# Kernel optimization log

Hardware: AMD Instinct MI355X
Metric: run time of the kernel (lower is better)

Reference implementation:

```python
import jax, jax.numpy as jnp
import numpy as np

B, N, H = 2048, 5, 5
IN, HID, OUT = 7, 2048, 512  # IN = 1 + c + c^2 with c = (H-1)//2 = 2


def setup_inputs() -> dict:
    key = jax.random.key(0)
    ks = jax.random.split(key, 7)
    k_in = 1.0 / np.sqrt(IN).astype(np.float32)
    k_h = 1.0 / np.sqrt(HID).astype(np.float32)
    return {
        "ins": jax.random.normal(ks[0], (B, N, H, H), jnp.float32),
        "w1": (jax.random.uniform(ks[1], (4, HID, IN), jnp.float32) - 0.5) * k_in,
        "b1": (jax.random.uniform(ks[2], (HID,), jnp.float32) - 0.5) * k_in,
        "w2": (jax.random.uniform(ks[3], (4, HID, HID), jnp.float32) - 0.5) * k_h,
        "b2": (jax.random.uniform(ks[4], (HID,), jnp.float32) - 0.5) * k_h,
        "w3": (jax.random.uniform(ks[5], (4, OUT, HID), jnp.float32) - 0.5) * k_h,
        "b3": (jax.random.uniform(ks[6], (OUT,), jnp.float32) - 0.5) * k_h,
        "ln_g": jnp.ones((HID,), jnp.float32),
        "ln_b": jnp.zeros((HID,), jnp.float32),
    }


def _rot90(x):
    # matches torch: x.flip(3).permute(0,1,3,2)
    return jnp.swapaxes(jnp.flip(x, axis=3), 2, 3)


def _orbit_stack(x):
    b, n = x.shape[0], x.shape[1]
    c = (x.shape[-1] - 1) // 2  # = 2 for H=5
    center = x[:, :, c, c]  # (B,N)
    parts = []
    xi = x
    for _ in range(4):  # fixed C4 group orbit, not a data loop
        parts.append(xi[:, :, :c, :c + 1].reshape(b, n, -1))  # (B,N,c+c^2)
        xi = _rot90(xi)
    orb = jnp.stack(parts, axis=-1)  # (B,N,c+c^2,4)
    cen = jnp.broadcast_to(center[..., None, None], (b, n, 1, 4))
    out = jnp.concatenate([cen, orb], axis=2)  # (B,N,n_orbits,4)
    return jnp.transpose(out, (0, 1, 3, 2))  # (B,N,4,n_orbits)


def _c4conv(w, bias, x):
    # block-circulant kernel: mat[g,h] = w[(h-g) % 4]
    mat = jnp.stack([jnp.roll(w, i, axis=0) for i in range(4)], axis=0)  # (4,4,out,in)
    return jnp.einsum('ghij,bnhj->bngi', mat, x) + bias


def _layernorm(x, g, b, eps=1e-5):
    m = jnp.mean(x, axis=-1, keepdims=True)
    v = jnp.mean(jnp.square(x - m), axis=-1, keepdims=True)
    return (x - m) / jnp.sqrt(v + eps) * g + b


def reference(ins, w1, b1, w2, b2, w3, b3, ln_g, ln_b):
    h = _orbit_stack(ins)                          # (B,N,4,7)
    h = jax.nn.relu(_c4conv(w1, b1, h))            # (B,N,4,HID)
    h = jax.nn.relu(_layernorm(_c4conv(w2, b2, h), ln_g, ln_b))
    return _c4conv(w3, b3, h)                      # (B,N,4,OUT)
```

## Files before the change

kernel.cpp:

```cpp
#include <hip/hip_runtime.h>
#include <stdint.h>


#define HID 2048
#define MROWS 10240

typedef float floatx4 __attribute__((ext_vector_type(4)));
typedef __bf16 bf16x8 __attribute__((ext_vector_type(8)));

__device__ __forceinline__ unsigned short f2bf(float f) {
  union { float f; unsigned int u; } v; v.f = f;
  unsigned int r = v.u + 0x7fffu + ((v.u >> 16) & 1u);
  return (unsigned short)(r >> 16);
}

template <int NO>
__global__ __launch_bounds__(256) void wtrans_kernel(const float* __restrict__ w,
                                                     unsigned short* __restrict__ W0s,
                                                     unsigned short* __restrict__ W2s,
                                                     unsigned short* __restrict__ Bc) {
  int idx = blockIdx.x * 256 + threadIdx.x;
  int i = idx >> 9, j4 = idx & 511;
  const float4* wp = (const float4*)w;
  float4 w0 = wp[0 * NO * 512 + i * 512 + j4];
  float4 w1 = wp[1 * NO * 512 + i * 512 + j4];
  float4 w2 = wp[2 * NO * 512 + i * 512 + j4];
  float4 w3 = wp[3 * NO * 512 + i * 512 + j4];
  ushort4 s0, s2, vr, vi, nvi;
#define DO(c)                                        \
  s0.c = f2bf(w0.c + w1.c + w2.c + w3.c);            \
  s2.c = f2bf(w0.c - w1.c + w2.c - w3.c);            \
  vr.c = f2bf(w0.c - w2.c);                          \
  vi.c = f2bf(w1.c - w3.c);                          \
  nvi.c = f2bf(-(w1.c - w3.c));
  DO(x) DO(y) DO(z) DO(w)
#undef DO
  ((ushort4*)W0s)[i * 512 + j4] = s0;
  ((ushort4*)W2s)[i * 512 + j4] = s2;
  ((ushort4*)Bc)[i * 1024 + j4] = vr;
  ((ushort4*)Bc)[i * 1024 + 512 + j4] = nvi;
  ((ushort4*)Bc)[(NO + i) * 1024 + j4] = vi;
  ((ushort4*)Bc)[(NO + i) * 1024 + 512 + j4] = vr;
}

__global__ __launch_bounds__(256) void layer1_kernel(const float* __restrict__ ins,
                                                     const float* __restrict__ w1,
                                                     const float* __restrict__ b1,
                                                     unsigned short* __restrict__ h1s,
                                                     int row0) {
  __shared__ float orbs[32][28];
  int t = threadIdx.x;
  int b0 = blockIdx.x * 32;
  int i = blockIdx.y * 256 + t;
  if (t < 32) {
    const float* x = ins + (size_t)(row0 + b0 + t) * 25;
    float v[25];
#pragma unroll
    for (int p = 0; p < 25; ++p) v[p] = x[p];
    float* o = orbs[t];
    o[0] = v[12]; o[7] = v[12]; o[14] = v[12]; o[21] = v[12];
#pragma unroll
    for (int r = 0; r < 2; ++r)
#pragma unroll
      for (int c = 0; c < 3; ++c) {
        int m = 1 + r * 3 + c;
        o[m]      = v[r * 5 + c];
        o[7 + m]  = v[c * 5 + (4 - r)];
        o[14 + m] = v[(4 - r) * 5 + (4 - c)];
        o[21 + m] = v[(4 - c) * 5 + r];
      }
  }
  __syncthreads();
  float w[4][7];
#pragma unroll
  for (int r = 0; r < 4; ++r)
#pragma unroll
    for (int j = 0; j < 7; ++j) w[r][j] = w1[(r * HID + i) * 7 + j];
  float bias = b1[i];
  for (int s = 0; s < 32; ++s) {
    float a[4] = {bias, bias, bias, bias};
#pragma unroll
    for (int hh = 0; hh < 4; ++hh)
#pragma unroll
      for (int j = 0; j < 7; ++j) {
        float ov = orbs[s][hh * 7 + j];
#pragma unroll
        for (int g = 0; g < 4; ++g) a[g] += w[(hh - g) & 3][j] * ov;
      }
    float h0 = fmaxf(a[0], 0.f), h1 = fmaxf(a[1], 0.f);
    float h2 = fmaxf(a[2], 0.f), h3 = fmaxf(a[3], 0.f);
    size_t base = (size_t)(b0 + s) * 8192 + i;
    h1s[base]        = f2bf(h0 + h1 + h2 + h3);
    h1s[base + 2048] = f2bf(h0 - h1 + h2 - h3);
    h1s[base + 4096] = f2bf(h0 - h2);
    h1s[base + 6144] = f2bf(h3 - h1);
  }
}

#define BM 128
#define BN 128
#define BK 64

__global__ __launch_bounds__(256) void gemm_spec(const unsigned short* __restrict__ A,
                                                 const unsigned short* __restrict__ B0,
                                                 const unsigned short* __restrict__ B1,
                                                 const unsigned short* __restrict__ B2,
                                                 float* __restrict__ C,
                                                 int s1, int s2, int N0, int ldc) {
  __shared__ __align__(16) unsigned short As[BM * BK];
  __shared__ __align__(16) unsigned short Bs[BN * BK];
  int tid = threadIdx.x;
  int wave = tid >> 6;
  int lane = tid & 63;
  int lane15 = lane & 15;
  int lane4 = lane >> 4;
  int m0 = blockIdx.y * BM;

  int bx = blockIdx.x;
  const unsigned short* Bp;
  int K, aoff, coff, nloc;
  if (bx < s1)      { Bp = B0; K = 2048; aoff = 0;    coff = 0;      nloc = bx * BN; }
  else if (bx < s2) { Bp = B1; K = 2048; aoff = 2048; coff = N0;     nloc = (bx - s1) * BN; }
  else              { Bp = B2; K = 4096; aoff = 4096; coff = 2 * N0; nloc = (bx - s2) * BN; }
  int ldb = K;

  int srow = wave * 8 + (lane >> 3);
  int scol = ((lane & 7) ^ (lane >> 3)) * 8;

  const unsigned short* Ag = A + (size_t)(m0 + srow) * 8192 + aoff + scol;
  const unsigned short* Bg = Bp + (size_t)(nloc + srow) * ldb + scol;

  int wm = (wave >> 1) * 64;
  int wn = (wave & 1) * 64;

  const floatx4 fz = {0.f, 0.f, 0.f, 0.f};
  floatx4 acc[4][4];
#pragma unroll
  for (int a = 0; a < 4; ++a)
#pragma unroll
    for (int b = 0; b < 4; ++b) acc[a][b] = fz;

  for (int k0 = 0; k0 < K; k0 += BK) {
#pragma unroll
    for (int q = 0; q < 4; ++q)
      __builtin_amdgcn_global_load_lds(
          (const __attribute__((address_space(1))) void*)(Ag + k0 + (size_t)q * 32 * 8192),
          (__attribute__((address_space(3))) void*)((char*)As + q * 4096 + wave * 1024),
          16, 0, 0);
#pragma unroll
    for (int q = 0; q < 4; ++q)
      __builtin_amdgcn_global_load_lds(
          (const __attribute__((address_space(1))) void*)(Bg + k0 + (size_t)q * 32 * ldb),
          (__attribute__((address_space(3))) void*)((char*)Bs + q * 4096 + wave * 1024),
          16, 0, 0);
    __syncthreads();
#pragma unroll
    for (int ks = 0; ks < 2; ++ks) {
      int chA = ((ks * 4 + lane4) ^ (lane15 & 7)) * 8;
      bf16x8 af[4], bfr[4];
#pragma unroll
      for (int mi = 0; mi < 4; ++mi)
        af[mi] = *(const bf16x8*)&As[(wm + mi * 16 + lane15) * BK + chA];
#pragma unroll
      for (int ni = 0; ni < 4; ++ni)
        bfr[ni] = *(const bf16x8*)&Bs[(wn + ni * 16 + lane15) * BK + chA];
#pragma unroll
      for (int mi = 0; mi < 4; ++mi)
#pragma unroll
        for (int ni = 0; ni < 4; ++ni)
          acc[mi][ni] = __builtin_amdgcn_mfma_f32_16x16x32_bf16(af[mi], bfr[ni], acc[mi][ni], 0, 0, 0);
    }
    __syncthreads();
  }

#pragma unroll
  for (int ni = 0; ni < 4; ++ni) {
    int col = coff + nloc + wn + ni * 16 + lane15;
#pragma unroll
    for (int mi = 0; mi < 4; ++mi) {
      int row = m0 + wm + mi * 16 + lane4 * 4;
#pragma unroll
      for (int r = 0; r < 4; ++r)
        C[(size_t)(row + r) * ldc + col] = acc[mi][ni][r];
    }
  }
}

__global__ __launch_bounds__(256) void ln_spec_kernel(const float* __restrict__ C2,
                                                      const float* __restrict__ b2,
                                                      const float* __restrict__ ln_g,
                                                      const float* __restrict__ ln_b,
                                                      unsigned short* __restrict__ h1s) {
  int t = threadIdx.x;
  size_t base = (size_t)blockIdx.x * 8192;
  const float4* p = (const float4*)(C2 + base);
  const float4* bp2 = (const float4*)b2;
  float4 y[4][2];
  float s[4] = {0, 0, 0, 0}, q[4] = {0, 0, 0, 0};
#pragma unroll
  for (int hl = 0; hl < 2; ++hl) {
    int j = hl * 256 + t;
    float4 v0 = p[j], v2 = p[512 + j], vr = p[1024 + j], vi = p[1536 + j];
    float4 bb = bp2[j];
#define DO(c)                                                   \
  {                                                             \
    float e0 = 0.25f * (v0.c + v2.c + 2.f * vr.c) + bb.c;       \
    float e1 = 0.25f * (v0.c - v2.c - 2.f * vi.c) + bb.c;       \
    float e2 = 0.25f * (v0.c + v2.c - 2.f * vr.c) + bb.c;       \
    float e3 = 0.25f * (v0.c - v2.c + 2.f * vi.c) + bb.c;       \
    y[0][hl].c = e0; y[1][hl].c = e1; y[2][hl].c = e2; y[3][hl].c = e3; \
    s[0] += e0; q[0] += e0 * e0; s[1] += e1; q[1] += e1 * e1;   \
    s[2] += e2; q[2] += e2 * e2; s[3] += e3; q[3] += e3 * e3;   \
  }
    DO(x) DO(y) DO(z) DO(w)
#undef DO
  }
#pragma unroll
  for (int off = 32; off > 0; off >>= 1)
#pragma unroll
    for (int g = 0; g < 4; ++g) {
      s[g] += __shfl_down(s[g], off, 64);
      q[g] += __shfl_down(q[g], off, 64);
    }
  __shared__ float rs[4][4], rq[4][4];
  int w = t >> 6, l = t & 63;
  if (l == 0)
#pragma unroll
    for (int g = 0; g < 4; ++g) { rs[w][g] = s[g]; rq[w][g] = q[g]; }
  __syncthreads();
  float mean[4], rstd[4];
#pragma unroll
  for (int g = 0; g < 4; ++g) {
    float ss = rs[0][g] + rs[1][g] + rs[2][g] + rs[3][g];
    float qq = rq[0][g] + rq[1][g] + rq[2][g] + rq[3][g];
    mean[g] = ss * (1.f / HID);
    float var = qq * (1.f / HID) - mean[g] * mean[g];
    rstd[g] = rsqrtf(var + 1e-5f);
  }
  const float4* gp = (const float4*)ln_g;
  const float4* lbp = (const float4*)ln_b;
#pragma unroll
  for (int hl = 0; hl < 2; ++hl) {
    int j = hl * 256 + t;
    float4 gg = gp[j], lb = lbp[j];
    ushort4 o[4];
#define DO(c)                                                               \
  {                                                                         \
    float h0 = fmaxf((y[0][hl].c - mean[0]) * rstd[0] * gg.c + lb.c, 0.f);  \
    float h1 = fmaxf((y[1][hl].c - mean[1]) * rstd[1] * gg.c + lb.c, 0.f);  \
    float h2 = fmaxf((y[2][hl].c - mean[2]) * rstd[2] * gg.c + lb.c, 0.f);  \
    float h3 = fmaxf((y[3][hl].c - mean[3]) * rstd[3] * gg.c + lb.c, 0.f);  \
    o[0].c = f2bf(h0 + h1 + h2 + h3);                                       \
    o[1].c = f2bf(h0 - h1 + h2 - h3);                                       \
    o[2].c = f2bf(h0 - h2);                                                 \
    o[3].c = f2bf(h3 - h1);                                                 \
  }
    DO(x) DO(y) DO(z) DO(w)
#undef DO
    size_t ob = (size_t)blockIdx.x * 8192;
#pragma unroll
    for (int pl = 0; pl < 4; ++pl)
      ((ushort4*)(h1s + ob + pl * 2048))[j] = o[pl];
  }
}

__global__ __launch_bounds__(256) void out_ep_kernel(const float* __restrict__ Z,
                                                     const float* __restrict__ b3,
                                                     float* __restrict__ out) {
  int e = blockIdx.x * 256 + threadIdx.x;
  int row = e >> 9, i = e & 511;
  size_t base = (size_t)row * 2048;
  float z0 = Z[base + i], z2 = Z[base + 512 + i];
  float zr = Z[base + 1024 + i], zi = Z[base + 1536 + i];
  float bv = b3[i];
  out[base + i]        = 0.25f * (z0 + z2 + 2.f * zr) + bv;
  out[base + 512 + i]  = 0.25f * (z0 - z2 - 2.f * zi) + bv;
  out[base + 1024 + i] = 0.25f * (z0 + z2 - 2.f * zr) + bv;
  out[base + 1536 + i] = 0.25f * (z0 - z2 + 2.f * zi) + bv;
}

extern "C" void kernel_launch(void* const* d_in, const int* in_sizes, int n_in,
                              void* d_out, int out_size, void* d_ws, size_t ws_size,
                              hipStream_t stream) {
  const float* ins = (const float*)d_in[0];
  const float* w1  = (const float*)d_in[1];
  const float* b1  = (const float*)d_in[2];
  const float* w2  = (const float*)d_in[3];
  const float* b2  = (const float*)d_in[4];
  const float* w3  = (const float*)d_in[5];
  const float* b3  = (const float*)d_in[6];
  const float* lng = (const float*)d_in[7];
  const float* lnb = (const float*)d_in[8];
  float* out = (float*)d_out;
  char* ws = (char*)d_ws;

  unsigned short* W0s2 = (unsigned short*)ws;
  unsigned short* W2s2 = W0s2 + 4194304;
  unsigned short* Bc2  = W2s2 + 4194304;
  unsigned short* W0s3 = Bc2 + 16777216;
  unsigned short* W2s3 = W0s3 + 1048576;
  unsigned short* Bc3  = W2s3 + 1048576;
  const size_t WT_BYTES = 62914560ull;
  char* chunk_base = ws + WT_BYTES;

  static const int Pcand[10] = {1, 2, 4, 5, 8, 10, 16, 20, 40, 80};
  int P = 80;
  for (int pi = 0; pi < 10; ++pi) {
    size_t mc = (size_t)MROWS / Pcand[pi];
    size_t need = WT_BYTES + mc * 8192 * 2 + mc * 8192 * 4 + 256;
    if (need <= ws_size) { P = Pcand[pi]; break; }
  }
  const int Mc = MROWS / P;
  unsigned short* h1s = (unsigned short*)chunk_base;
  float*          C2  = (float*)(chunk_base + (size_t)Mc * 8192 * 2);
  float*          Z   = C2;

  wtrans_kernel<2048><<<4096, 256, 0, stream>>>(w2, W0s2, W2s2, Bc2);
  wtrans_kernel<512><<<1024, 256, 0, stream>>>(w3, W0s3, W2s3, Bc3);

  for (int c = 0; c < P; ++c) {
    int row0 = c * Mc;
    layer1_kernel<<<dim3(Mc / 32, 8), 256, 0, stream>>>(ins, w1, b1, h1s, row0);
    gemm_spec<<<dim3(64, Mc / 128), 256, 0, stream>>>(h1s, W0s2, W2s2, Bc2, C2,
                                                      16, 32, 2048, 8192);
    ln_spec_kernel<<<Mc, 256, 0, stream>>>(C2, b2, lng, lnb, h1s);
    gemm_spec<<<dim3(16, Mc / 128), 256, 0, stream>>>(h1s, W0s3, W2s3, Bc3, Z,
                                                      4, 8, 512, 2048);
    out_ep_kernel<<<Mc * 2, 256, 0, stream>>>(Z, b3, out + (size_t)row0 * 2048);
  }
}
```

Measured before the change: 1.198 ms.

## Store layer-2 GEMM output as bf16 and swizzle GEMM tile order into panels

The second-layer GEMM now writes its intermediate result in bf16 instead of fp32, and the layernorm kernel reads bf16 and converts back to float. This halves the intermediate write and read traffic and the workspace size, which may also allow fewer chunks. GEMM blocks are also remapped into column panels of width 8 so blocks sharing B tiles run close together, aiming for better L2 reuse. The bf16 rounding before layernorm adds error in exchange.

```diff
diff --git a/kernel.cpp b/kernel.cpp
--- a/kernel.cpp
+++ b/kernel.cpp
@@ -12,6 +12,10 @@
   union { float f; unsigned int u; } v; v.f = f;
   unsigned int r = v.u + 0x7fffu + ((v.u >> 16) & 1u);
   return (unsigned short)(r >> 16);
+}
+__device__ __forceinline__ float bf2f(unsigned short s) {
+  union { unsigned int u; float f; } v; v.u = ((unsigned int)s) << 16;
+  return v.f;
 }
 
 template <int NO>
@@ -100,12 +104,14 @@
 #define BM 128
 #define BN 128
 #define BK 64
+#define PW 8
 
 __global__ __launch_bounds__(256) void gemm_spec(const unsigned short* __restrict__ A,
                                                  const unsigned short* __restrict__ B0,
                                                  const unsigned short* __restrict__ B1,
                                                  const unsigned short* __restrict__ B2,
-                                                 float* __restrict__ C,
+                                                 float* __restrict__ Cf,
+                                                 unsigned short* __restrict__ Cb,
                                                  int s1, int s2, int N0, int ldc) {
   __shared__ __align__(16) unsigned short As[BM * BK];
   __shared__ __align__(16) unsigned short Bs[BN * BK];
@@ -114,14 +120,19 @@
   int lane = tid & 63;
   int lane15 = lane & 15;
   int lane4 = lane >> 4;
-  int m0 = blockIdx.y * BM;
-
-  int bx = blockIdx.x;
+
+  int flat = blockIdx.y * gridDim.x + blockIdx.x;
+  int panel = flat / (PW * gridDim.y);
+  int rem = flat % (PW * gridDim.y);
+  int mt = rem / PW;
+  int nt = panel * PW + rem % PW;
+  int m0 = mt * BM;
+
   const unsigned short* Bp;
   int K, aoff, coff, nloc;
-  if (bx < s1)      { Bp = B0; K = 2048; aoff = 0;    coff = 0;      nloc = bx * BN; }
-  else if (bx < s2) { Bp = B1; K = 2048; aoff = 2048; coff = N0;     nloc = (bx - s1) * BN; }
-  else              { Bp = B2; K = 4096; aoff = 4096; coff = 2 * N0; nloc = (bx - s2) * BN; }
+  if (nt < s1)      { Bp = B0; K = 2048; aoff = 0;    coff = 0;      nloc = nt * BN; }
+  else if (nt < s2) { Bp = B1; K = 2048; aoff = 2048; coff = N0;     nloc = (nt - s1) * BN; }
+  else              { Bp = B2; K = 4096; aoff = 4096; coff = 2 * N0; nloc = (nt - s2) * BN; }
   int ldb = K;
 
   int srow = wave * 8 + (lane >> 3);
@@ -179,35 +190,43 @@
 #pragma unroll
     for (int mi = 0; mi < 4; ++mi) {
       int row = m0 + wm + mi * 16 + lane4 * 4;
-#pragma unroll
-      for (int r = 0; r < 4; ++r)
-        C[(size_t)(row + r) * ldc + col] = acc[mi][ni][r];
+      if (Cb) {
+#pragma unroll
+        for (int r = 0; r < 4; ++r)
+          Cb[(size_t)(row + r) * ldc + col] = f2bf(acc[mi][ni][r]);
+      } else {
+#pragma unroll
+        for (int r = 0; r < 4; ++r)
+          Cf[(size_t)(row + r) * ldc + col] = acc[mi][ni][r];
+      }
     }
   }
 }
 
-__global__ __launch_bounds__(256) void ln_spec_kernel(const float* __restrict__ C2,
+__global__ __launch_bounds__(256) void ln_spec_kernel(const unsigned short* __restrict__ C2,
                                                       const float* __restrict__ b2,
                                                       const float* __restrict__ ln_g,
                                                       const float* __restrict__ ln_b,
                                                       unsigned short* __restrict__ h1s) {
   int t = threadIdx.x;
   size_t base = (size_t)blockIdx.x * 8192;
-  const float4* p = (const float4*)(C2 + base);
+  const ushort4* p = (const ushort4*)(C2 + base);
   const float4* bp2 = (const float4*)b2;
   float4 y[4][2];
   float s[4] = {0, 0, 0, 0}, q[4] = {0, 0, 0, 0};
 #pragma unroll
   for (int hl = 0; hl < 2; ++hl) {
     int j = hl * 256 + t;
-    float4 v0 = p[j], v2 = p[512 + j], vr = p[1024 + j], vi = p[1536 + j];
+    ushort4 u0 = p[j], u2 = p[512 + j], ur = p[1024 + j], ui = p[1536 + j];
     float4 bb = bp2[j];
 #define DO(c)                                                   \
   {                                                             \
-    float e0 = 0.25f * (v0.c + v2.c + 2.f * vr.c) + bb.c;       \
-    float e1 = 0.25f * (v0.c - v2.c - 2.f * vi.c) + bb.c;       \
-    float e2 = 0.25f * (v0.c + v2.c - 2.f * vr.c) + bb.c;       \
-    float e3 = 0.25f * (v0.c - v2.c + 2.f * vi.c) + bb.c;       \
+    float v0 = bf2f(u0.c), v2 = bf2f(u2.c);                     \
+    float vr = bf2f(ur.c), vi = bf2f(ui.c);                     \
+    float e0 = 0.25f * (v0 + v2 + 2.f * vr) + bb.c;             \
+    float e1 = 0.25f * (v0 - v2 - 2.f * vi) + bb.c;             \
+    float e2 = 0.25f * (v0 + v2 - 2.f * vr) + bb.c;             \
+    float e3 = 0.25f * (v0 - v2 + 2.f * vi) + bb.c;             \
     y[0][hl].c = e0; y[1][hl].c = e1; y[2][hl].c = e2; y[3][hl].c = e3; \
     s[0] += e0; q[0] += e0 * e0; s[1] += e1; q[1] += e1 * e1;   \
     s[2] += e2; q[2] += e2 * e2; s[3] += e3; q[3] += e3 * e3;   \
@@ -307,13 +326,13 @@
   int P = 80;
   for (int pi = 0; pi < 10; ++pi) {
     size_t mc = (size_t)MROWS / Pcand[pi];
-    size_t need = WT_BYTES + mc * 8192 * 2 + mc * 8192 * 4 + 256;
+    size_t need = WT_BYTES + mc * 8192 * 2 * 2 + 256;
     if (need <= ws_size) { P = Pcand[pi]; break; }
   }
   const int Mc = MROWS / P;
   unsigned short* h1s = (unsigned short*)chunk_base;
-  float*          C2  = (float*)(chunk_base + (size_t)Mc * 8192 * 2);
-  float*          Z   = C2;
+  unsigned short* C2  = (unsigned short*)(chunk_base + (size_t)Mc * 8192 * 2);
+  float*          Z   = (float*)C2;
 
   wtrans_kernel<2048><<<4096, 256, 0, stream>>>(w2, W0s2, W2s2, Bc2);
   wtrans_kernel<512><<<1024, 256, 0, stream>>>(w3, W0s3, W2s3, Bc3);
@@ -321,10 +340,10 @@
   for (int c = 0; c < P; ++c) {
     int row0 = c * Mc;
     layer1_kernel<<<dim3(Mc / 32, 8), 256, 0, stream>>>(ins, w1, b1, h1s, row0);
-    gemm_spec<<<dim3(64, Mc / 128), 256, 0, stream>>>(h1s, W0s2, W2s2, Bc2, C2,
+    gemm_spec<<<dim3(64, Mc / 128), 256, 0, stream>>>(h1s, W0s2, W2s2, Bc2, nullptr, C2,
                                                       16, 32, 2048, 8192);
     ln_spec_kernel<<<Mc, 256, 0, stream>>>(C2, b2, lng, lnb, h1s);
-    gemm_spec<<<dim3(16, Mc / 128), 256, 0, stream>>>(h1s, W0s3, W2s3, Bc3, Z,
+    gemm_spec<<<dim3(16, Mc / 128), 256, 0, stream>>>(h1s, W0s3, W2s3, Bc3, Z, nullptr,
                                                       4, 8, 512, 2048);
     out_ep_kernel<<<Mc * 2, 256, 0, stream>>>(Z, b3, out + (size_t)row0 * 2048);
   }
```

After: 1.182 ms. About the same (-1.3%).
